# Kernel tuning notes

Hardware: AMD Instinct MI355X
Metric: run time of the kernel (lower is better)

## Reference

```python
import jax, jax.numpy as jnp
import numpy as np
from functools import reduce

# 6x6 open-boundary PEPS, bond dim D=4, physical dim 2, boundary contraction
# from ymin with projector compression to CHI=8, projectors perturbed by a
# 2-layer MLP of the spin configuration (eta = 1e-3), then full contraction.
Lx, Ly, D, PHYS = 6, 6, 4, 2
CHI = 8
NHID = 64
ETA = 1e-3
NSITES = Lx * Ly
BATCH = 1024


def _proj_shapes():
    # Static propagation of projector tensor shapes (mirrors the sweep below).
    u = [1] + [D] * (Lx - 1)
    d = [D] * (Lx - 1) + [1]
    shapes = []
    for j in range(1, Ly - 1):
        nu = [u[i] * (1 if i == 0 else D) for i in range(Lx)]
        nd = [d[i] * (1 if i == Lx - 1 else D) for i in range(Lx)]
        for i in range(Lx - 1):
            m = nd[i]
            k1 = min(nu[i] * D, m)
            k2 = min(D * nd[i + 1], m)
            cb = min(CHI, k1, k2)
            shapes += [(m, cb), (m, cb)]
            nd[i] = cb
            nu[i + 1] = cb
        u, d = nu, nd
    return shapes


PROJ_SHAPES = _proj_shapes()
PROJ_LEN = sum(m * c for m, c in PROJ_SHAPES)  # == 6400


def _site(T, xi, i, j):
    # select physical index; axes of result: (up, right, down, left)
    t = jnp.take(T[i, j], xi[i * Ly + j], axis=-1)
    if i == 0:
        t = t[:1]          # lattice top edge: up bond is trivial
    if i == Lx - 1:
        t = t[:, :, :1]    # lattice bottom edge: down bond is trivial
    return t


def _sweep(A, projs):
    # boundary MPS from column 0; B[i] axes: (u, r, d)
    B = [A[i][0][:, :, :, 0] for i in range(Lx)]
    out = [] if projs is None else None
    p = 0
    for j in range(1, Ly - 1):
        Bn = []
        for i in range(Lx):
            t = A[i][j]  # (a, R, b, l)
            nt = jnp.einsum('uxd,aRbx->uaRdb', B[i], t)
            u_, a_, R_, d_, b_ = nt.shape
            Bn.append(nt.reshape(u_ * a_, R_, d_ * b_))
        for i in range(Lx - 1):
            Tt, Tb = Bn[i], Bn[i + 1]
            m = Tt.shape[-1]
            if projs is None:
                mt = Tt.reshape(-1, m)        # (ut*R, m)
                mb = Tb.reshape(m, -1)        # (m, R*db)
                R1 = jnp.linalg.qr(mt, mode='r')     # (k1, m)
                R2 = jnp.linalg.qr(mb.T, mode='r')   # (k2, m)
                U, S, Vh = jnp.linalg.svd(R1 @ R2.T, full_matrices=False)
                cb = min(CHI, S.shape[-1])
                sinv = 1.0 / jnp.sqrt(S[:cb] + 1e-12)
                Pd = (R2.T @ Vh[:cb].T) * sinv  # (m, cb): top tensor's down bond
                Pu = (R1.T @ U[:, :cb]) * sinv  # (m, cb): bottom tensor's up bond
                out += [Pd, Pu]
            else:
                Pd, Pu = projs[p], projs[p + 1]
                p += 2
            Bn[i] = jnp.einsum('uRm,mc->uRc', Tt, Pd)
            Bn[i + 1] = jnp.einsum('mRd,mc->cRd', Tb, Pu)
        B = Bn
    return B, out


def _finalize(B, A):
    Cs = []
    for i in range(Lx):
        t = A[i][Ly - 1][:, 0]  # (a, b, l): right bond is trivial
        c = jnp.einsum('uxd,abx->uadb', B[i], t)
        ua, aa, dd, bb = c.shape
        Cs.append(c.reshape(ua * aa, dd * bb))
    return reduce(jnp.matmul, Cs)[0, 0]


def _mlp(xf, W1, b1, W2, b2):
    h = jax.nn.relu(xf @ W1.T + b1)
    return h @ W2.T + b2


def _amp_single(T, W1, b1, W2, b2, xi):
    A = [[_site(T, xi, i, j) for j in range(Ly)] for i in range(Lx)]
    # pass 1: compute data-dependent projectors
    _, plist = _sweep(A, None)
    vec = jnp.concatenate([pp.reshape(-1) for pp in plist])
    vec = vec + _mlp(xi.astype(jnp.float32), W1, b1, W2, b2) * ETA
    # unpack perturbed projectors
    newp, ptr = [], 0
    for pp in plist:
        n = pp.size
        newp.append(vec[ptr:ptr + n].reshape(pp.shape))
        ptr += n
    # pass 2: contract the full network with the perturbed projectors
    B, _ = _sweep(A, newp)
    return _finalize(B, A)


def setup_inputs() -> dict:
    key = jax.random.key(0)
    ks = jax.random.split(key, 6)
    T = jax.random.normal(ks[0], (Lx, Ly, D, D, D, D, PHYS), dtype=jnp.float32) * 0.5
    W1 = jax.random.normal(ks[1], (NHID, NSITES), dtype=jnp.float32) / np.sqrt(NSITES).astype(np.float32)
    b1 = jnp.zeros((NHID,), dtype=jnp.float32)
    W2 = jax.random.normal(ks[2], (PROJ_LEN, NHID), dtype=jnp.float32) / np.sqrt(NHID).astype(np.float32)
    b2 = jnp.zeros((PROJ_LEN,), dtype=jnp.float32)
    x = jax.random.randint(ks[3], (BATCH, NSITES), 0, PHYS, dtype=jnp.int32)
    return {"T": T, "W1": W1, "b1": b1, "W2": W2, "b2": b2, "x": x}


def reference(T, W1, b1, W2, b2, x):
    return jax.vmap(lambda xi: _amp_single(T, W1, b1, W2, b2, xi))(x)
```

## Files before the change

kernel.cpp:

```cpp
#include <hip/hip_runtime.h>

#define BS 256

__device__ const int g_uprev[2][6] = {{1,4,4,4,4,4},{1,4,8,8,8,4}};
__device__ const int g_dprev[2][6] = {{4,4,4,4,4,1},{4,8,8,8,4,1}};
__device__ const int g_mtab[2][5]  = {{16,16,16,16,16},{16,32,32,32,16}};
__device__ const int g_cbtab[5]    = {4,8,8,8,4};
__device__ const int g_ucurtab[5]  = {1,4,8,8,8};
__device__ const int g_dntab[2][5] = {{16,16,16,16,1},{32,32,32,16,1}};
__device__ const int g_path[2][5]  = {{0,0,1,1,2},{0,0,0,0,2}};
__device__ const int g_offtab[4][5]= {{0,128,384,640,896},
                                      {1024,1152,1664,2176,2688},
                                      {2816,2944,3456,3968,4480},
                                      {4608,4736,5248,5760,6272}};
__device__ const int g_ufin[6] = {1,4,8,8,8,4};
__device__ const int g_dfin[6] = {4,8,8,8,4,1};

__global__ __launch_bounds__(256) void mlp_kernel(
    const float* __restrict__ W1, const float* __restrict__ b1,
    const float* __restrict__ W2, const float* __restrict__ b2,
    const int* __restrict__ x, float* __restrict__ proj)
{
  __shared__ float hbuf[8][64];
  const int tid = threadIdx.x;
  const int s0 = blockIdx.x << 3;
  for (int e = tid; e < 512; e += 256) {
    const int sl = e >> 6, hh = e & 63;
    const int* xr = x + (s0 + sl) * 36;
    const float* wr = W1 + hh * 36;
    float acc = b1[hh];
    #pragma unroll
    for (int t = 0; t < 36; ++t) acc += wr[t] * (float)xr[t];
    hbuf[sl][hh] = fmaxf(acc, 0.0f);
  }
  __syncthreads();
  for (int k = tid; k < 6400; k += 256) {
    const float4* wr = (const float4*)(W2 + (size_t)k * 64);
    float acc[8];
    #pragma unroll
    for (int s2 = 0; s2 < 8; ++s2) acc[s2] = 0.0f;
    #pragma unroll
    for (int c = 0; c < 16; ++c) {
      const float4 w = wr[c];
      #pragma unroll
      for (int s2 = 0; s2 < 8; ++s2) {
        const float4 hv = ((const float4*)hbuf[s2])[c];
        acc[s2] += w.x * hv.x + w.y * hv.y + w.z * hv.z + w.w * hv.w;
      }
    }
    const float bb = b2[k];
    #pragma unroll
    for (int s2 = 0; s2 < 8; ++s2)
      proj[(size_t)(s0 + s2) * 6400 + k] = 0.001f * (acc[s2] + bb);
  }
}

__device__ __forceinline__ void jrot(float app, float aqq, float apq, float& c, float& sn) {
  c = 1.0f; sn = 0.0f;
  if (fabsf(apq) > 1e-36f + 1e-12f * (fabsf(app) + fabsf(aqq))) {
    const float tau = (aqq - app) * 0.5f * __builtin_amdgcn_rcpf(apq);
    const float t = copysignf(1.0f, tau) *
                    __builtin_amdgcn_rcpf(fabsf(tau) + __builtin_amdgcn_sqrtf(1.0f + tau * tau));
    c = __builtin_amdgcn_rsqf(1.0f + t * t);
    sn = t * c;
  }
}

__device__ __forceinline__ int seatof(int i, int n) {
  return (i == n - 1) ? 0 : ((i == 0) ? 1 : ((i < (n >> 1)) ? (2 * i) : (2 * (n - 1 - i) + 1)));
}

__device__ __forceinline__ int sgshift(int s, int np) {
  if (s == 0) return 0;
  if (s & 1) return (s == 2 * np - 1) ? (2 * np - 2) : (s + 2);
  return (s == 2) ? 1 : (s - 2);
}

template<int N>
__device__ void jacobi_pb(float* __restrict__ H, float* __restrict__ V, int tid)
{
  constexpr int NP = N / 2;
  constexpr int NM1 = N - 1;
  constexpr int NL = (N == 32) ? 5 : ((N == 16) ? 4 : 2);
  constexpr int NVMAX = (N == 32) ? 2 : 1;
  constexpr int MAXSW = (N == 32) ? 5 : ((N == 16) ? 5 : 3);
  for (int e = tid; e < N * N; e += BS) {
    const int r = e >> NL, c = e & (N - 1);
    const int i0 = (c == 0) ? NM1 : ((c == 1) ? 0 : ((c & 1) ? (NM1 - (c >> 1)) : (c >> 1)));
    V[r * 36 + c] = (r == i0) ? 1.0f : 0.0f;
  }
  __syncthreads();
  const int cp = tid & (NP - 1);
  const bool hact = (N == 32) ? true : ((N == 16) ? (tid < 64) : (tid < 4));
  const bool vact = (N == 32) ? true : ((N == 16) ? (tid < 128) : (tid < 8));
  const int q0 = 2 * cp, q1 = q0 + 1;
  const int d0 = sgshift(q0, NP), d1 = sgshift(q1, NP);
  const int rt = (N == 32) ? (tid >> 4) : ((N == 16) ? (tid >> 3) : (tid >> 1));
  const int r0 = 2 * rt, r1 = r0 + 1;
  const int e0 = sgshift(r0, NP), e1 = sgshift(r1, NP);
  int vr[NVMAX];
  #pragma unroll
  for (int vi = 0; vi < NVMAX; ++vi)
    vr[vi] = ((N == 32) ? (tid >> 4) : ((N == 16) ? (tid >> 3) : (tid >> 1))) + NP * vi;

  for (int sw = 0; sw < MAXSW; ++sw) {
    for (int rd = 0; rd < NM1; ++rd) {
      const float2 dg = *(const float2*)(H + q0 * 36 + q0);
      const float aqq = H[q1 * 36 + q1];
      float cc_, cs_;
      jrot(dg.x, aqq, dg.y, cc_, cs_);
      float o00, o01, o10, o11;
      if (hact) {
        const float cr_ = __shfl(cc_, rt);
        const float sr_ = __shfl(cs_, rt);
        const float2 rA = *(const float2*)(H + r0 * 36 + q0);
        const float2 rB = *(const float2*)(H + r1 * 36 + q0);
        const float t1 = cr_ * rA.x - sr_ * rB.x, t2 = cr_ * rA.y - sr_ * rB.y;
        const float u1 = sr_ * rA.x + cr_ * rB.x, u2 = sr_ * rA.y + cr_ * rB.y;
        o00 = cc_ * t1 - cs_ * t2; o01 = cs_ * t1 + cc_ * t2;
        o10 = cc_ * u1 - cs_ * u2; o11 = cs_ * u1 + cc_ * u2;
      }
      float v0[NVMAX], v1[NVMAX];
      #pragma unroll
      for (int vi = 0; vi < NVMAX; ++vi) {
        if (vi == 0 && !vact) continue;
        const float2 vv = *(const float2*)(V + vr[vi] * 36 + q0);
        v0[vi] = cc_ * vv.x - cs_ * vv.y;
        v1[vi] = cs_ * vv.x + cc_ * vv.y;
      }
      __syncthreads();
      if (hact) {
        H[e0 * 36 + d0] = o00; H[e0 * 36 + d1] = o01;
        H[e1 * 36 + d0] = o10; H[e1 * 36 + d1] = o11;
      }
      #pragma unroll
      for (int vi = 0; vi < NVMAX; ++vi) {
        if (vi == 0 && !vact) continue;
        V[vr[vi] * 36 + d0] = v0[vi];
        V[vr[vi] * 36 + d1] = v1[vi];
      }
      __syncthreads();
    }
  }
}

__device__ __forceinline__ void gram_cols(float* __restrict__ G, const float* __restrict__ A,
                                          int nrows, int mcols, bool init, int tid)
{
  const int q4 = mcols >> 2;
  const int q4log = (mcols == 32) ? 3 : 2;
  const int nel = mcols * q4;
  const float4* A4 = (const float4*)A;
  float4* G4 = (float4*)G;
  for (int e = tid; e < nel; e += BS) {
    const int c2q = e & (q4 - 1);
    const int c1 = e >> q4log;
    float ax = 0.f, ay = 0.f, az = 0.f, aw = 0.f;
    for (int r = 0; r < nrows; ++r) {
      const float a1 = A[r * 36 + c1];
      const float4 a2 = A4[r * 9 + c2q];
      ax += a1 * a2.x; ay += a1 * a2.y; az += a1 * a2.z; aw += a1 * a2.w;
    }
    float4* gp = G4 + c1 * 9 + c2q;
    if (init) { float4 o; o.x = ax; o.y = ay; o.z = az; o.w = aw; *gp = o; }
    else { float4 o = *gp; o.x += ax; o.y += ay; o.z += az; o.w += aw; *gp = o; }
  }
  __syncthreads();
}

__device__ __forceinline__ void absorb_T(const float* __restrict__ Tg, const float* __restrict__ poolS,
    float* __restrict__ BIGT, float* __restrict__ ATile, const int* __restrict__ xi,
    int i1, int j, int U, int Dd, int rr0, int rr1, int tid)
{
  const int bd = (i1 == 5) ? 1 : 4;
  const int dbw = Dd * bd;
  const int mt_ = U * 4;
  const int ph = xi[i1 * 6 + j];
  const float* tb = Tg + (size_t)(i1 * 6 + j) * 512;
  for (int e = tid; e < 256; e += BS) ATile[e] = tb[e * 2 + ph];
  __syncthreads();
  const int mlog = (mt_ == 32) ? 5 : 4;
  const int dblog = 31 - __clz(dbw);
  const int bdlog = (bd == 4) ? 2 : 0;
  const int nel = mt_ * dbw * (rr1 - rr0);
  for (int e = tid; e < nel; e += BS) {
    const int ua = e & (mt_ - 1);
    const int db = (e >> mlog) & (dbw - 1);
    const int rr = rr0 + (e >> (mlog + dblog));
    const int u = ua >> 2, a = ua & 3;
    const int d_ = db >> bdlog, b = db & (bd - 1);
    const float* op = poolS + u * 33 + d_;
    const float4 av = *(const float4*)(ATile + a * 64 + rr * 16 + b * 4);
    BIGT[((rr - rr0) * dbw + db) * 36 + ua] = op[0] * av.x + op[8] * av.y + op[16] * av.z + op[24] * av.w;
  }
  __syncthreads();
}

__global__ __launch_bounds__(256, 4) void peps_kernel(
    const float* __restrict__ Tg, const int* __restrict__ x,
    float* __restrict__ proj, float* __restrict__ out)
{
  __shared__ __align__(16) float pool[6 * 264];
  __shared__ __align__(16) float CUR[1152];
  __shared__ __align__(16) float BIGT[2304];
  __shared__ __align__(16) float GbM[1152];
  __shared__ __align__(16) float TM[1152];
  __shared__ __align__(16) float GM[1152];
  __shared__ __align__(16) float ATile[256];
  __shared__ __align__(16) float PdL[256], PuL[256];
  __shared__ float red[4];
  __shared__ int isel[8];
  __shared__ float sinvv[8], sdiv[8];
  __shared__ int xi[36];
  __shared__ float vvec[36], vvec2[36];

  const int s = blockIdx.x;
  const int tid = threadIdx.x;
  if (tid < 36) xi[tid] = x[s * 36 + tid];
  __syncthreads();

  for (int sweep = 0; sweep < 2; ++sweep) {
    for (int i2 = 0; i2 < 6; ++i2) {
      const int ad = (i2 == 0) ? 1 : 4, bd = (i2 == 5) ? 1 : 4;
      const int bdlog = (bd == 4) ? 2 : 0;
      const int ph = xi[i2 * 6];
      const float* tb = Tg + (size_t)(i2 * 6) * 512;
      const int nel = ad * 4 * bd;
      for (int e = tid; e < nel; e += BS) {
        const int b = e & (bd - 1);
        const int rr = (e >> bdlog) & 3;
        const int a = e >> (bdlog + 2);
        pool[i2 * 264 + a * 33 + rr * 8 + b] = tb[(a * 64 + rr * 16 + b * 4) * 2 + ph];
      }
    }
    __syncthreads();

    for (int j = 1; j <= 4; ++j) {
      const int jj = (j > 1) ? 1 : 0;
      {
        const int ph = xi[j];
        const float* tb = Tg + (size_t)j * 512;
        for (int e = tid; e < 256; e += BS) ATile[e] = tb[e * 2 + ph];
        __syncthreads();
        for (int e = tid; e < 64; e += BS) {
          const int db = e & 15;
          const int rr = e >> 4;
          const int d_ = db >> 2, b = db & 3;
          const float* op = pool + d_;
          const float4 av = *(const float4*)(ATile + rr * 16 + b * 4);
          CUR[rr * 36 + db] = op[0] * av.x + op[8] * av.y + op[16] * av.z + op[24] * av.w;
        }
        __syncthreads();
      }

      for (int i = 0; i < 5; ++i) {
        const int m = g_mtab[jj][i], cb = g_cbtab[i], ucur = g_ucurtab[i], dn = g_dntab[jj][i];
        const int p = ucur * 4, path = g_path[jj][i];
        const int U1 = g_uprev[jj][i + 1], Dd1 = g_dprev[jj][i + 1];
        const bool two = (dn == 32);
        const int cblog = (cb == 8) ? 3 : 2;
        const int mq4 = m >> 2;
        float* projb = proj + (size_t)s * 6400 + g_offtab[j - 1][i];

        if (sweep == 0) {
          if (path == 2) {
            absorb_T(Tg, pool + (i + 1) * 264, BIGT, ATile, xi, i + 1, j, U1, Dd1, 0, 4, tid);
            gram_cols(GbM, CUR, p, m, true, tid);
            for (int e = tid; e < 64; e += BS) {
              const int r = e & 3, k = e >> 2;
              float acc = 0.f;
              const float4* G4 = (const float4*)GbM;
              const float4* B4 = (const float4*)BIGT;
              for (int lq = 0; lq < 4; ++lq) {
                const float4 g = G4[k * 9 + lq], b = B4[r * 9 + lq];
                acc += g.x * b.x + g.y * b.y + g.z * b.z + g.w * b.w;
              }
              TM[k * 36 + r] = acc;
            }
            __syncthreads();
            for (int e = tid; e < 16; e += BS) {
              const int c = e & 3, r = e >> 2;
              float acc = 0.f;
              for (int k = 0; k < 16; ++k) acc += BIGT[r * 36 + k] * TM[k * 36 + c];
              GM[seatof(r, 4) * 36 + seatof(c, 4)] = acc;
            }
            __syncthreads();
            jacobi_pb<4>(GM, TM + 576, tid);
          } else if (path == 0) {
            if (!two) {
              absorb_T(Tg, pool + (i + 1) * 264, BIGT, ATile, xi, i + 1, j, U1, Dd1, 0, 4, tid);
              gram_cols(GbM, BIGT, 4 * dn, m, true, tid);
            } else {
              absorb_T(Tg, pool + (i + 1) * 264, BIGT, ATile, xi, i + 1, j, U1, Dd1, 0, 2, tid);
              gram_cols(GbM, BIGT, 2 * dn, m, true, tid);
              absorb_T(Tg, pool + (i + 1) * 264, BIGT, ATile, xi, i + 1, j, U1, Dd1, 2, 4, tid);
              gram_cols(GbM, BIGT, 2 * dn, m, false, tid);
            }
            const int q4log = (m == 32) ? 3 : 2;
            for (int e = tid; e < p * mq4; e += BS) {
              const int lq = e & (mq4 - 1), pr = e >> q4log;
              float ax = 0.f, ay = 0.f, az = 0.f, aw = 0.f;
              const float4* G4 = (const float4*)GbM;
              for (int k = 0; k < m; ++k) {
                const float a1 = CUR[pr * 36 + k];
                const float4 g = G4[k * 9 + lq];
                ax += a1 * g.x; ay += a1 * g.y; az += a1 * g.z; aw += a1 * g.w;
              }
              float4 o; o.x = ax; o.y = ay; o.z = az; o.w = aw;
              ((float4*)TM)[pr * 9 + lq] = o;
            }
            __syncthreads();
            const int plog = (p == 32) ? 5 : ((p == 16) ? 4 : 2);
            for (int e = tid; e < p * p; e += BS) {
              const int pc = e & (p - 1), pr = e >> plog;
              float acc = 0.f;
              const float4* T4 = (const float4*)TM;
              const float4* C4 = (const float4*)CUR;
              for (int lq = 0; lq < mq4; ++lq) {
                const float4 t = T4[pr * 9 + lq], c = C4[pc * 9 + lq];
                acc += t.x * c.x + t.y * c.y + t.z * c.z + t.w * c.w;
              }
              GM[seatof(pr, p) * 36 + seatof(pc, p)] = acc;
            }
            __syncthreads();
            if (p == 4)       jacobi_pb<4>(GM, TM, tid);
            else if (p == 16) jacobi_pb<16>(GM, TM, tid);
            else              jacobi_pb<32>(GM, TM, tid);
          } else {
            absorb_T(Tg, pool + (i + 1) * 264, BIGT, ATile, xi, i + 1, j, U1, Dd1, 0, 4, tid);
            gram_cols(GbM + 576, CUR, p, m, true, tid);
            gram_cols(GbM, BIGT, 4 * dn, m, true, tid);
            if (tid < 64) {
              float v_ = (tid < 16) ? GbM[tid * 37] : -3.0e38f;
              for (int mk = 32; mk; mk >>= 1) v_ = fmaxf(v_, __shfl_xor(v_, mk));
              if (tid == 0) red[0] = v_;
            }
            __syncthreads();
            const float thr = 1e-10f * red[0] + 1e-35f;
            for (int k = 0; k < 16; ++k) {
              const float dk = GbM[k * 37];
              const float rs = (dk > thr) ? (1.0f / sqrtf(dk)) : 0.0f;
              if (tid < 16) TM[k * 36 + tid] = GbM[k * 36 + tid] * rs;
              __syncthreads();
              const int rows = 15 - k;
              for (int e = tid; e < rows * 16; e += BS) {
                const int ii = k + 1 + (e >> 4), jc = e & 15;
                GbM[ii * 36 + jc] -= TM[k * 36 + ii] * TM[k * 36 + jc];
              }
              __syncthreads();
            }
            for (int e = tid; e < 64; e += BS) {
              const int jq = e & 3, k = e >> 2;
              float ax = 0.f, ay = 0.f, az = 0.f, aw = 0.f;
              const float4* Gt4 = (const float4*)(GbM + 576);
              for (int l = 0; l < 16; ++l) {
                const float r2 = TM[k * 36 + l];
                const float4 g = Gt4[l * 9 + jq];
                ax += r2 * g.x; ay += r2 * g.y; az += r2 * g.z; aw += r2 * g.w;
              }
              float4 o; o.x = ax; o.y = ay; o.z = az; o.w = aw;
              ((float4*)(TM + 576))[k * 9 + jq] = o;
            }
            __syncthreads();
            for (int e = tid; e < 256; e += BS) {
              const int k2 = e & 15, k = e >> 4;
              float acc = 0.f;
              const float4* T14 = (const float4*)(TM + 576);
              const float4* R24 = (const float4*)TM;
              for (int lq = 0; lq < 4; ++lq) {
                const float4 t = T14[k * 9 + lq], r = R24[k2 * 9 + lq];
                acc += t.x * r.x + t.y * r.y + t.z * r.z + t.w * r.w;
              }
              GM[seatof(k, 16) * 36 + seatof(k2, 16)] = acc;
            }
            __syncthreads();
            jacobi_pb<16>(GM, TM + 576, tid);
          }

          const int N = (path == 2) ? 4 : ((path == 1) ? 16 : p);
          if (tid < 64) {
            float v_ = (tid < N) ? GM[tid * 37] : -3.0e38f;
            int ix = tid;
            for (int t = 0; t < cb; ++t) {
              float bv = v_; int bi = ix;
              for (int mk = 32; mk; mk >>= 1) {
                const float ov = __shfl_xor(bv, mk);
                const int oi = __shfl_xor(bi, mk);
                if (ov > bv || (ov == bv && oi < bi)) { bv = ov; bi = oi; }
              }
              if (tid == 0) isel[t] = bi;
              if (ix == bi) v_ = -3.0e38f;
            }
          }
          __syncthreads();
          if (tid < cb) {
            const float lam = GM[isel[tid] * 37];
            const float s_ = sqrtf(fmaxf(lam, 0.0f));
            sinvv[tid] = 1.0f / sqrtf(s_ + 1e-12f);
            sdiv[tid]  = 1.0f / fmaxf(s_, 1e-25f);
          }
          __syncthreads();

          if (path == 0) {
            for (int e = tid; e < m * cb; e += BS) {
              const int k = e & (cb - 1), mrow = e >> cblog;
              const int a = isel[k];
              float acc = 0.f;
              for (int pr = 0; pr < p; ++pr) acc += CUR[pr * 36 + mrow] * TM[pr * 36 + a];
              PuL[mrow * 8 + k] = acc * sinvv[k];
            }
            __syncthreads();
            for (int e = tid; e < m * cb; e += BS) {
              const int k = e & (cb - 1), mrow = e >> cblog;
              float acc = 0.f;
              for (int l = 0; l < m; ++l) acc += GbM[mrow * 36 + l] * PuL[l * 8 + k];
              PdL[mrow * 8 + k] = acc * sdiv[k];
            }
            __syncthreads();
          } else if (path == 2) {
            for (int e = tid; e < m * cb; e += BS) {
              const int k = e & (cb - 1), mrow = e >> cblog;
              const int a = isel[k];
              float acc = 0.f;
              for (int r = 0; r < 4; ++r) acc += BIGT[r * 36 + mrow] * TM[576 + r * 36 + a];
              PdL[mrow * 8 + k] = acc * sinvv[k];
            }
            __syncthreads();
            for (int e = tid; e < m * cb; e += BS) {
              const int k = e & (cb - 1), mrow = e >> cblog;
              float acc = 0.f;
              for (int l = 0; l < m; ++l) acc += GbM[mrow * 36 + l] * PdL[l * 8 + k];
              PuL[mrow * 8 + k] = acc * sdiv[k];
            }
            __syncthreads();
          } else {
            for (int e = tid; e < m * cb; e += BS) {
              const int k = e & (cb - 1), mrow = e >> cblog;
              const int a = isel[k];
              float acc = 0.f;
              for (int t = 0; t < 16; ++t) acc += TM[t * 36 + mrow] * TM[576 + t * 36 + a];
              PdL[mrow * 8 + k] = acc * sinvv[k];
            }
            __syncthreads();
            for (int e = tid; e < m * cb; e += BS) {
              const int k = e & (cb - 1), mrow = e >> cblog;
              float acc = 0.f;
              for (int l = 0; l < m; ++l) acc += GbM[576 + mrow * 36 + l] * PdL[l * 8 + k];
              PuL[mrow * 8 + k] = acc * sdiv[k];
            }
            __syncthreads();
          }
          for (int e = tid; e < m * cb; e += BS)
            projb[e] += PdL[(e >> cblog) * 8 + (e & (cb - 1))];
          for (int e = tid; e < m * cb; e += BS)
            projb[m * cb + e] += PuL[(e >> cblog) * 8 + (e & (cb - 1))];
        } else {
          for (int e = tid; e < m * cb; e += BS)
            PdL[(e >> cblog) * 8 + (e & (cb - 1))] = projb[e];
          for (int e = tid; e < m * cb; e += BS)
            PuL[(e >> cblog) * 8 + (e & (cb - 1))] = projb[m * cb + e];
          __syncthreads();
          if (!two) absorb_T(Tg, pool + (i + 1) * 264, BIGT, ATile, xi, i + 1, j, U1, Dd1, 0, 4, tid);
          else      absorb_T(Tg, pool + (i + 1) * 264, BIGT, ATile, xi, i + 1, j, U1, Dd1, 2, 4, tid);
        }

        {
          const int nel = ucur * 4 * cb;
          const float4* C4 = (const float4*)CUR;
          for (int e = tid; e < nel; e += BS) {
            const int cc = e & (cb - 1);
            const int rr = (e >> cblog) & 3;
            const int u = e >> (cblog + 2);
            const int row = u * 4 + rr;
            float acc = 0.f;
            for (int mq = 0; mq < mq4; ++mq) {
              const float4 cv = C4[row * 9 + mq];
              acc += cv.x * PdL[(mq * 4 + 0) * 8 + cc] + cv.y * PdL[(mq * 4 + 1) * 8 + cc]
                   + cv.z * PdL[(mq * 4 + 2) * 8 + cc] + cv.w * PdL[(mq * 4 + 3) * 8 + cc];
            }
            pool[i * 264 + u * 33 + rr * 8 + cc] = acc;
          }
          __syncthreads();

          const int dnlog = 31 - __clz(dn);
          auto bn1 = [&](int rr0, int nloc) {
            const int ne2 = cb * nloc * dn;
            const float4* B4 = (const float4*)BIGT;
            for (int e = tid; e < ne2; e += BS) {
              const int dd = e & (dn - 1);
              const int t = e >> dnlog;
              const int rrL = t & (nloc - 1);
              const int cc = t >> ((nloc == 4) ? 2 : 1);
              const int row = rrL * dn + dd;
              float acc = 0.f;
              for (int mq = 0; mq < mq4; ++mq) {
                const float4 bv = B4[row * 9 + mq];
                acc += bv.x * PuL[(mq * 4 + 0) * 8 + cc] + bv.y * PuL[(mq * 4 + 1) * 8 + cc]
                     + bv.z * PuL[(mq * 4 + 2) * 8 + cc] + bv.w * PuL[(mq * 4 + 3) * 8 + cc];
              }
              if (i < 4) CUR[(cc * 4 + rr0 + rrL) * 36 + dd] = acc;
              else       pool[5 * 264 + cc * 33 + (rr0 + rrL) * 8] = acc;
            }
            __syncthreads();
          };
          if (!two) {
            bn1(0, 4);
          } else {
            bn1(2, 2);
            absorb_T(Tg, pool + (i + 1) * 264, BIGT, ATile, xi, i + 1, j, U1, Dd1, 0, 2, tid);
            bn1(0, 2);
          }
        }
      }
    }

    if (sweep == 1) {
      if (tid == 0) vvec[0] = 1.0f;
      __syncthreads();
      for (int i = 0; i < 6; ++i) {
        const int ad = (i == 0) ? 1 : 4, bd = (i == 5) ? 1 : 4;
        const int adlog = (ad == 4) ? 2 : 0, bdlog = (bd == 4) ? 2 : 0;
        const int rows = g_ufin[i] * ad, cols = g_dfin[i] * bd;
        const int clog = 31 - __clz(cols);
        const int ph = xi[i * 6 + 5];
        const float* tb = Tg + (size_t)(i * 6 + 5) * 512;
        for (int e = tid; e < 256; e += BS) ATile[e] = tb[e * 2 + ph];
        __syncthreads();
        for (int e = tid; e < rows * cols; e += BS) {
          const int col = e & (cols - 1);
          const int ua = e >> clog;
          const int u = ua >> adlog, a = ua & (ad - 1);
          const int d_ = col >> bdlog, b = col & (bd - 1);
          const float* fb = pool + i * 264 + u * 33 + d_;
          const float4 av = *(const float4*)(ATile + a * 64 + b * 4);
          GM[ua * 36 + col] = fb[0] * av.x + fb[8] * av.y + fb[16] * av.z + fb[24] * av.w;
        }
        __syncthreads();
        if (tid < cols) {
          float acc = 0.f;
          for (int r_ = 0; r_ < rows; ++r_) acc += vvec[r_] * GM[r_ * 36 + tid];
          vvec2[tid] = acc;
        }
        __syncthreads();
        if (tid < cols) vvec[tid] = vvec2[tid];
        __syncthreads();
      }
      if (tid == 0) out[s] = vvec[0];
    }
  }
}

extern "C" void kernel_launch(void* const* d_in, const int* in_sizes, int n_in,
                              void* d_out, int out_size, void* d_ws, size_t ws_size,
                              hipStream_t stream) {
  const float* Tg = (const float*)d_in[0];
  const float* W1 = (const float*)d_in[1];
  const float* b1 = (const float*)d_in[2];
  const float* W2 = (const float*)d_in[3];
  const float* b2 = (const float*)d_in[4];
  const int*   x  = (const int*)d_in[5];
  float* out = (float*)d_out;
  float* proj = (float*)d_ws;
  (void)in_sizes; (void)n_in; (void)out_size; (void)ws_size;

  mlp_kernel<<<dim3(128), dim3(256), 0, stream>>>(W1, b1, W2, b2, x, proj);
  peps_kernel<<<dim3(1024), dim3(256), 0, stream>>>(Tg, x, proj, out);
}
```

Baseline: 1.360 ms.

## Process two samples per block to amortize barriers and fill idle lanes

```diff
diff --git a/kernel.cpp b/kernel.cpp
--- a/kernel.cpp
+++ b/kernel.cpp
@@ -1,6 +1,9 @@
 #include <hip/hip_runtime.h>
 
 #define BS 256
+#define SS 1152
+#define PSS 1584
+#define BSS 2304
 
 __device__ const int g_uprev[2][6] = {{1,4,4,4,4,4},{1,4,8,8,8,4}};
 __device__ const int g_dprev[2][6] = {{4,4,4,4,4,1},{4,8,8,8,4,1}};
@@ -69,7 +72,6 @@
 __device__ __forceinline__ int seatof(int i, int n) {
   return (i == n - 1) ? 0 : ((i == 0) ? 1 : ((i < (n >> 1)) ? (2 * i) : (2 * (n - 1 - i) + 1)));
 }
-
 __device__ __forceinline__ int sgshift(int s, int np) {
   if (s == 0) return 0;
   if (s & 1) return (s == 2 * np - 1) ? (2 * np - 2) : (s + 2);
@@ -77,91 +79,140 @@
 }
 
 template<int N>
-__device__ void jacobi_pb(float* __restrict__ H, float* __restrict__ V, int tid)
+__device__ void jacobi_pb(float* __restrict__ Hb, float* __restrict__ Vb, int tid)
 {
   constexpr int NP = N / 2;
   constexpr int NM1 = N - 1;
   constexpr int NL = (N == 32) ? 5 : ((N == 16) ? 4 : 2);
-  constexpr int NVMAX = (N == 32) ? 2 : 1;
   constexpr int MAXSW = (N == 32) ? 5 : ((N == 16) ? 5 : 3);
-  for (int e = tid; e < N * N; e += BS) {
+  for (int e2 = tid; e2 < 2 * N * N; e2 += BS) {
+    const int sm = (e2 >= N * N) ? 1 : 0;
+    const int e = e2 - sm * N * N;
     const int r = e >> NL, c = e & (N - 1);
     const int i0 = (c == 0) ? NM1 : ((c == 1) ? 0 : ((c & 1) ? (NM1 - (c >> 1)) : (c >> 1)));
-    V[r * 36 + c] = (r == i0) ? 1.0f : 0.0f;
+    Vb[sm * SS + r * 36 + c] = (r == i0) ? 1.0f : 0.0f;
   }
   __syncthreads();
   const int cp = tid & (NP - 1);
-  const bool hact = (N == 32) ? true : ((N == 16) ? (tid < 64) : (tid < 4));
-  const bool vact = (N == 32) ? true : ((N == 16) ? (tid < 128) : (tid < 8));
   const int q0 = 2 * cp, q1 = q0 + 1;
   const int d0 = sgshift(q0, NP), d1 = sgshift(q1, NP);
-  const int rt = (N == 32) ? (tid >> 4) : ((N == 16) ? (tid >> 3) : (tid >> 1));
-  const int r0 = 2 * rt, r1 = r0 + 1;
-  const int e0 = sgshift(r0, NP), e1 = sgshift(r1, NP);
-  int vr[NVMAX];
-  #pragma unroll
-  for (int vi = 0; vi < NVMAX; ++vi)
-    vr[vi] = ((N == 32) ? (tid >> 4) : ((N == 16) ? (tid >> 3) : (tid >> 1))) + NP * vi;
-
-  for (int sw = 0; sw < MAXSW; ++sw) {
-    for (int rd = 0; rd < NM1; ++rd) {
-      const float2 dg = *(const float2*)(H + q0 * 36 + q0);
-      const float aqq = H[q1 * 36 + q1];
-      float cc_, cs_;
-      jrot(dg.x, aqq, dg.y, cc_, cs_);
-      float o00, o01, o10, o11;
-      if (hact) {
-        const float cr_ = __shfl(cc_, rt);
-        const float sr_ = __shfl(cs_, rt);
-        const float2 rA = *(const float2*)(H + r0 * 36 + q0);
-        const float2 rB = *(const float2*)(H + r1 * 36 + q0);
-        const float t1 = cr_ * rA.x - sr_ * rB.x, t2 = cr_ * rA.y - sr_ * rB.y;
-        const float u1 = sr_ * rA.x + cr_ * rB.x, u2 = sr_ * rA.y + cr_ * rB.y;
-        o00 = cc_ * t1 - cs_ * t2; o01 = cs_ * t1 + cc_ * t2;
-        o10 = cc_ * u1 - cs_ * u2; o11 = cs_ * u1 + cc_ * u2;
+
+  if (N == 32) {
+    const int rt = tid >> 4;
+    const int r0 = 2 * rt, r1 = r0 + 1;
+    const int e0 = sgshift(r0, NP), e1 = sgshift(r1, NP);
+    const int vrow0 = rt, vrow1 = rt + 16;
+    for (int sw = 0; sw < MAXSW; ++sw)
+      for (int rd = 0; rd < NM1; ++rd) {
+        float c0, s0, c1, s1;
+        { const float2 dg = *(const float2*)(Hb + q0 * 36 + q0);
+          jrot(dg.x, Hb[q1 * 36 + q1], dg.y, c0, s0); }
+        { const float2 dg = *(const float2*)(Hb + SS + q0 * 36 + q0);
+          jrot(dg.x, Hb[SS + q1 * 36 + q1], dg.y, c1, s1); }
+        const float cr0 = __shfl(c0, rt), sr0 = __shfl(s0, rt);
+        const float cr1 = __shfl(c1, rt), sr1 = __shfl(s1, rt);
+        float o[2][4], va[2][2], vb[2][2];
+        #pragma unroll
+        for (int sm = 0; sm < 2; ++sm) {
+          const float cc_ = sm ? c1 : c0, cs_ = sm ? s1 : s0;
+          const float cr_ = sm ? cr1 : cr0, sr_ = sm ? sr1 : sr0;
+          const float* H = Hb + sm * SS;
+          const float2 rA = *(const float2*)(H + r0 * 36 + q0);
+          const float2 rB = *(const float2*)(H + r1 * 36 + q0);
+          const float t1 = cr_ * rA.x - sr_ * rB.x, t2 = cr_ * rA.y - sr_ * rB.y;
+          const float u1 = sr_ * rA.x + cr_ * rB.x, u2 = sr_ * rA.y + cr_ * rB.y;
+          o[sm][0] = cc_ * t1 - cs_ * t2; o[sm][1] = cs_ * t1 + cc_ * t2;
+          o[sm][2] = cc_ * u1 - cs_ * u2; o[sm][3] = cs_ * u1 + cc_ * u2;
+          const float* V = Vb + sm * SS;
+          const float2 v0 = *(const float2*)(V + vrow0 * 36 + q0);
+          const float2 v1 = *(const float2*)(V + vrow1 * 36 + q0);
+          va[sm][0] = cc_ * v0.x - cs_ * v0.y; va[sm][1] = cs_ * v0.x + cc_ * v0.y;
+          vb[sm][0] = cc_ * v1.x - cs_ * v1.y; vb[sm][1] = cs_ * v1.x + cc_ * v1.y;
+        }
+        __syncthreads();
+        #pragma unroll
+        for (int sm = 0; sm < 2; ++sm) {
+          float* H = Hb + sm * SS;
+          H[e0 * 36 + d0] = o[sm][0]; H[e0 * 36 + d1] = o[sm][1];
+          H[e1 * 36 + d0] = o[sm][2]; H[e1 * 36 + d1] = o[sm][3];
+          float* V = Vb + sm * SS;
+          V[vrow0 * 36 + d0] = va[sm][0]; V[vrow0 * 36 + d1] = va[sm][1];
+          V[vrow1 * 36 + d0] = vb[sm][0]; V[vrow1 * 36 + d1] = vb[sm][1];
+        }
+        __syncthreads();
       }
-      float v0[NVMAX], v1[NVMAX];
-      #pragma unroll
-      for (int vi = 0; vi < NVMAX; ++vi) {
-        if (vi == 0 && !vact) continue;
-        const float2 vv = *(const float2*)(V + vr[vi] * 36 + q0);
-        v0[vi] = cc_ * vv.x - cs_ * vv.y;
-        v1[vi] = cs_ * vv.x + cc_ * vv.y;
+  } else {
+    const int hsm = (N == 16) ? ((tid >> 6) & 1) : ((tid >> 2) & 1);
+    const bool hact = (N == 16) ? (tid < 128) : (tid < 8);
+    const int rt = (N == 16) ? ((tid >> 3) & 7) : ((tid >> 1) & 1);
+    const int r0 = 2 * rt, r1 = r0 + 1;
+    const int e0 = sgshift(r0, NP), e1 = sgshift(r1, NP);
+    const int vsm = (N == 16) ? (tid >> 7) : ((tid >> 3) & 1);
+    const bool vact = (N == 16) ? true : (tid < 16);
+    const int vrow = (N == 16) ? ((tid >> 3) & 15) : ((tid >> 1) & 3);
+    for (int sw = 0; sw < MAXSW; ++sw)
+      for (int rd = 0; rd < NM1; ++rd) {
+        float c0, s0, c1, s1;
+        { const float2 dg = *(const float2*)(Hb + q0 * 36 + q0);
+          jrot(dg.x, Hb[q1 * 36 + q1], dg.y, c0, s0); }
+        { const float2 dg = *(const float2*)(Hb + SS + q0 * 36 + q0);
+          jrot(dg.x, Hb[SS + q1 * 36 + q1], dg.y, c1, s1); }
+        const float cr0 = __shfl(c0, rt), sr0 = __shfl(s0, rt);
+        const float cr1 = __shfl(c1, rt), sr1 = __shfl(s1, rt);
+        float o0, o1, o2, o3, w0, w1;
+        if (hact) {
+          const float cc_ = hsm ? c1 : c0, cs_ = hsm ? s1 : s0;
+          const float cr_ = hsm ? cr1 : cr0, sr_ = hsm ? sr1 : sr0;
+          const float* H = Hb + hsm * SS;
+          const float2 rA = *(const float2*)(H + r0 * 36 + q0);
+          const float2 rB = *(const float2*)(H + r1 * 36 + q0);
+          const float t1 = cr_ * rA.x - sr_ * rB.x, t2 = cr_ * rA.y - sr_ * rB.y;
+          const float u1 = sr_ * rA.x + cr_ * rB.x, u2 = sr_ * rA.y + cr_ * rB.y;
+          o0 = cc_ * t1 - cs_ * t2; o1 = cs_ * t1 + cc_ * t2;
+          o2 = cc_ * u1 - cs_ * u2; o3 = cs_ * u1 + cc_ * u2;
+        }
+        if (vact) {
+          const float cc_ = vsm ? c1 : c0, cs_ = vsm ? s1 : s0;
+          const float2 vv = *(const float2*)(Vb + vsm * SS + vrow * 36 + q0);
+          w0 = cc_ * vv.x - cs_ * vv.y;
+          w1 = cs_ * vv.x + cc_ * vv.y;
+        }
+        __syncthreads();
+        if (hact) {
+          float* H = Hb + hsm * SS;
+          H[e0 * 36 + d0] = o0; H[e0 * 36 + d1] = o1;
+          H[e1 * 36 + d0] = o2; H[e1 * 36 + d1] = o3;
+        }
+        if (vact) {
+          float* V = Vb + vsm * SS;
+          V[vrow * 36 + d0] = w0;
+          V[vrow * 36 + d1] = w1;
+        }
+        __syncthreads();
       }
-      __syncthreads();
-      if (hact) {
-        H[e0 * 36 + d0] = o00; H[e0 * 36 + d1] = o01;
-        H[e1 * 36 + d0] = o10; H[e1 * 36 + d1] = o11;
-      }
-      #pragma unroll
-      for (int vi = 0; vi < NVMAX; ++vi) {
-        if (vi == 0 && !vact) continue;
-        V[vr[vi] * 36 + d0] = v0[vi];
-        V[vr[vi] * 36 + d1] = v1[vi];
-      }
-      __syncthreads();
-    }
   }
 }
 
 __device__ __forceinline__ void gram_cols(float* __restrict__ G, const float* __restrict__ A,
-                                          int nrows, int mcols, bool init, int tid)
+                                          int as_, int nrows, int mcols, bool init, int tid)
 {
   const int q4 = mcols >> 2;
   const int q4log = (mcols == 32) ? 3 : 2;
   const int nel = mcols * q4;
-  const float4* A4 = (const float4*)A;
-  float4* G4 = (float4*)G;
-  for (int e = tid; e < nel; e += BS) {
+  for (int e2 = tid; e2 < 2 * nel; e2 += BS) {
+    const int sm = (e2 >= nel) ? 1 : 0;
+    const int e = e2 - sm * nel;
+    const float* As = A + sm * as_;
+    float* Gs = G + sm * SS;
     const int c2q = e & (q4 - 1);
     const int c1 = e >> q4log;
     float ax = 0.f, ay = 0.f, az = 0.f, aw = 0.f;
     for (int r = 0; r < nrows; ++r) {
-      const float a1 = A[r * 36 + c1];
-      const float4 a2 = A4[r * 9 + c2q];
+      const float a1 = As[r * 36 + c1];
+      const float4 a2 = *(const float4*)(As + r * 36 + c2q * 4);
       ax += a1 * a2.x; ay += a1 * a2.y; az += a1 * a2.z; aw += a1 * a2.w;
     }
-    float4* gp = G4 + c1 * 9 + c2q;
+    float4* gp = (float4*)(Gs + c1 * 36 + c2q * 4);
     if (init) { float4 o; o.x = ax; o.y = ay; o.z = az; o.w = aw; *gp = o; }
     else { float4 o = *gp; o.x += ax; o.y += ay; o.z += az; o.w += aw; *gp = o; }
   }
@@ -175,62 +226,69 @@
   const int bd = (i1 == 5) ? 1 : 4;
   const int dbw = Dd * bd;
   const int mt_ = U * 4;
-  const int ph = xi[i1 * 6 + j];
   const float* tb = Tg + (size_t)(i1 * 6 + j) * 512;
-  for (int e = tid; e < 256; e += BS) ATile[e] = tb[e * 2 + ph];
+  for (int e2 = tid; e2 < 512; e2 += BS) {
+    const int sm = e2 >> 8, e = e2 & 255;
+    ATile[sm * 256 + e] = tb[e * 2 + xi[sm * 36 + i1 * 6 + j]];
+  }
   __syncthreads();
   const int mlog = (mt_ == 32) ? 5 : 4;
   const int dblog = 31 - __clz(dbw);
   const int bdlog = (bd == 4) ? 2 : 0;
   const int nel = mt_ * dbw * (rr1 - rr0);
-  for (int e = tid; e < nel; e += BS) {
+  for (int e2 = tid; e2 < 2 * nel; e2 += BS) {
+    const int sm = (e2 >= nel) ? 1 : 0;
+    const int e = e2 - sm * nel;
     const int ua = e & (mt_ - 1);
     const int db = (e >> mlog) & (dbw - 1);
     const int rr = rr0 + (e >> (mlog + dblog));
     const int u = ua >> 2, a = ua & 3;
     const int d_ = db >> bdlog, b = db & (bd - 1);
-    const float* op = poolS + u * 33 + d_;
-    const float4 av = *(const float4*)(ATile + a * 64 + rr * 16 + b * 4);
-    BIGT[((rr - rr0) * dbw + db) * 36 + ua] = op[0] * av.x + op[8] * av.y + op[16] * av.z + op[24] * av.w;
+    const float* op = poolS + sm * PSS + u * 33 + d_;
+    const float4 av = *(const float4*)(ATile + sm * 256 + a * 64 + rr * 16 + b * 4);
+    BIGT[sm * BSS + ((rr - rr0) * dbw + db) * 36 + ua] =
+        op[0] * av.x + op[8] * av.y + op[16] * av.z + op[24] * av.w;
   }
   __syncthreads();
 }
 
-__global__ __launch_bounds__(256, 4) void peps_kernel(
+__global__ __launch_bounds__(256, 2) void peps_kernel(
     const float* __restrict__ Tg, const int* __restrict__ x,
     float* __restrict__ proj, float* __restrict__ out)
 {
-  __shared__ __align__(16) float pool[6 * 264];
-  __shared__ __align__(16) float CUR[1152];
-  __shared__ __align__(16) float BIGT[2304];
-  __shared__ __align__(16) float GbM[1152];
-  __shared__ __align__(16) float TM[1152];
-  __shared__ __align__(16) float GM[1152];
-  __shared__ __align__(16) float ATile[256];
-  __shared__ __align__(16) float PdL[256], PuL[256];
-  __shared__ float red[4];
-  __shared__ int isel[8];
-  __shared__ float sinvv[8], sdiv[8];
-  __shared__ int xi[36];
-  __shared__ float vvec[36], vvec2[36];
-
-  const int s = blockIdx.x;
+  __shared__ __align__(16) float pool[2 * PSS];
+  __shared__ __align__(16) float CUR[2 * SS];
+  __shared__ __align__(16) float BIGT[2 * BSS];
+  __shared__ __align__(16) float GbM[2 * SS];
+  __shared__ __align__(16) float TM[2 * SS];
+  __shared__ __align__(16) float GM[2 * SS];
+  __shared__ __align__(16) float ATile[2 * 256];
+  __shared__ __align__(16) float PdL[2 * 256], PuL[2 * 256];
+  __shared__ float red[2];
+  __shared__ int isel[2 * 8];
+  __shared__ float sinvv[2 * 8], sdiv[2 * 8];
+  __shared__ int xi[2 * 36];
+  __shared__ float vvec[2 * 36], vvec2[2 * 36];
+
+  const int s0 = blockIdx.x * 2;
   const int tid = threadIdx.x;
-  if (tid < 36) xi[tid] = x[s * 36 + tid];
+  if (tid < 72) xi[tid] = x[s0 * 36 + tid];
   __syncthreads();
 
   for (int sweep = 0; sweep < 2; ++sweep) {
     for (int i2 = 0; i2 < 6; ++i2) {
       const int ad = (i2 == 0) ? 1 : 4, bd = (i2 == 5) ? 1 : 4;
       const int bdlog = (bd == 4) ? 2 : 0;
-      const int ph = xi[i2 * 6];
       const float* tb = Tg + (size_t)(i2 * 6) * 512;
       const int nel = ad * 4 * bd;
-      for (int e = tid; e < nel; e += BS) {
+      for (int e2 = tid; e2 < 2 * nel; e2 += BS) {
+        const int sm = (e2 >= nel) ? 1 : 0;
+        const int e = e2 - sm * nel;
+        const int ph = xi[sm * 36 + i2 * 6];
         const int b = e & (bd - 1);
         const int rr = (e >> bdlog) & 3;
         const int a = e >> (bdlog + 2);
-        pool[i2 * 264 + a * 33 + rr * 8 + b] = tb[(a * 64 + rr * 16 + b * 4) * 2 + ph];
+        pool[sm * PSS + i2 * 264 + a * 33 + rr * 8 + b] = tb[(a * 64 + rr * 16 + b * 4) * 2 + ph];
       }
     }
     __syncthreads();
@@ -238,17 +296,20 @@
     for (int j = 1; j <= 4; ++j) {
       const int jj = (j > 1) ? 1 : 0;
       {
-        const int ph = xi[j];
         const float* tb = Tg + (size_t)j * 512;
-        for (int e = tid; e < 256; e += BS) ATile[e] = tb[e * 2 + ph];
-        __syncthreads();
-        for (int e = tid; e < 64; e += BS) {
-          const int db = e & 15;
-          const int rr = e >> 4;
+        for (int e2 = tid; e2 < 512; e2 += BS) {
+          const int sm = e2 >> 8, e = e2 & 255;
+          ATile[sm * 256 + e] = tb[e * 2 + xi[sm * 36 + j]];
+        }
+        __syncthreads();
+        for (int e2 = tid; e2 < 128; e2 += BS) {
+          const int sm = e2 >= 64 ? 1 : 0;
+          const int e = e2 & 63;
+          const int db = e & 15, rr = e >> 4;
           const int d_ = db >> 2, b = db & 3;
-          const float* op = pool + d_;
-          const float4 av = *(const float4*)(ATile + rr * 16 + b * 4);
-          CUR[rr * 36 + db] = op[0] * av.x + op[8] * av.y + op[16] * av.z + op[24] * av.w;
+          const float* op = pool + sm * PSS + d_;
+          const float4 av = *(const float4*)(ATile + sm * 256 + rr * 16 + b * 4);
+          CUR[sm * SS + rr * 36 + db] = op[0] * av.x + op[8] * av.y + op[16] * av.z + op[24] * av.w;
         }
         __syncthreads();
       }
@@ -260,67 +321,75 @@
         const bool two = (dn == 32);
         const int cblog = (cb == 8) ? 3 : 2;
         const int mq4 = m >> 2;
-        float* projb = proj + (size_t)s * 6400 + g_offtab[j - 1][i];
+        const int offv = g_offtab[j - 1][i];
 
         if (sweep == 0) {
           if (path == 2) {
             absorb_T(Tg, pool + (i + 1) * 264, BIGT, ATile, xi, i + 1, j, U1, Dd1, 0, 4, tid);
-            gram_cols(GbM, CUR, p, m, true, tid);
-            for (int e = tid; e < 64; e += BS) {
+            gram_cols(GbM, CUR, SS, p, m, true, tid);
+            for (int e2 = tid; e2 < 128; e2 += BS) {
+              const int sm = e2 >= 64 ? 1 : 0;
+              const int e = e2 & 63;
               const int r = e & 3, k = e >> 2;
               float acc = 0.f;
-              const float4* G4 = (const float4*)GbM;
-              const float4* B4 = (const float4*)BIGT;
               for (int lq = 0; lq < 4; ++lq) {
-                const float4 g = G4[k * 9 + lq], b = B4[r * 9 + lq];
+                const float4 g = *(const float4*)(GbM + sm * SS + k * 36 + lq * 4);
+                const float4 b = *(const float4*)(BIGT + sm * BSS + r * 36 + lq * 4);
                 acc += g.x * b.x + g.y * b.y + g.z * b.z + g.w * b.w;
               }
-              TM[k * 36 + r] = acc;
-            }
-            __syncthreads();
-            for (int e = tid; e < 16; e += BS) {
+              TM[sm * SS + k * 36 + r] = acc;
+            }
+            __syncthreads();
+            for (int e2 = tid; e2 < 32; e2 += BS) {
+              const int sm = e2 >= 16 ? 1 : 0;
+              const int e = e2 & 15;
               const int c = e & 3, r = e >> 2;
               float acc = 0.f;
-              for (int k = 0; k < 16; ++k) acc += BIGT[r * 36 + k] * TM[k * 36 + c];
-              GM[seatof(r, 4) * 36 + seatof(c, 4)] = acc;
+              for (int k = 0; k < 16; ++k)
+                acc += BIGT[sm * BSS + r * 36 + k] * TM[sm * SS + k * 36 + c];
+              GM[sm * SS + seatof(r, 4) * 36 + seatof(c, 4)] = acc;
             }
             __syncthreads();
             jacobi_pb<4>(GM, TM + 576, tid);
           } else if (path == 0) {
             if (!two) {
               absorb_T(Tg, pool + (i + 1) * 264, BIGT, ATile, xi, i + 1, j, U1, Dd1, 0, 4, tid);
-              gram_cols(GbM, BIGT, 4 * dn, m, true, tid);
+              gram_cols(GbM, BIGT, BSS, 4 * dn, m, true, tid);
             } else {
               absorb_T(Tg, pool + (i + 1) * 264, BIGT, ATile, xi, i + 1, j, U1, Dd1, 0, 2, tid);
-              gram_cols(GbM, BIGT, 2 * dn, m, true, tid);
+              gram_cols(GbM, BIGT, BSS, 2 * dn, m, true, tid);
               absorb_T(Tg, pool + (i + 1) * 264, BIGT, ATile, xi, i + 1, j, U1, Dd1, 2, 4, tid);
-              gram_cols(GbM, BIGT, 2 * dn, m, false, tid);
+              gram_cols(GbM, BIGT, BSS, 2 * dn, m, false, tid);
             }
             const int q4log = (m == 32) ? 3 : 2;
-            for (int e = tid; e < p * mq4; e += BS) {
+            const int nel1 = p * mq4;
+            for (int e2 = tid; e2 < 2 * nel1; e2 += BS) {
+              const int sm = (e2 >= nel1) ? 1 : 0;
+              const int e = e2 - sm * nel1;
               const int lq = e & (mq4 - 1), pr = e >> q4log;
               float ax = 0.f, ay = 0.f, az = 0.f, aw = 0.f;
-              const float4* G4 = (const float4*)GbM;
               for (int k = 0; k < m; ++k) {
-                const float a1 = CUR[pr * 36 + k];
-                const float4 g = G4[k * 9 + lq];
+                const float a1 = CUR[sm * SS + pr * 36 + k];
+                const float4 g = *(const float4*)(GbM + sm * SS + k * 36 + lq * 4);
                 ax += a1 * g.x; ay += a1 * g.y; az += a1 * g.z; aw += a1 * g.w;
               }
               float4 o; o.x = ax; o.y = ay; o.z = az; o.w = aw;
-              ((float4*)TM)[pr * 9 + lq] = o;
+              *(float4*)(TM + sm * SS + pr * 36 + lq * 4) = o;
             }
             __syncthreads();
             const int plog = (p == 32) ? 5 : ((p == 16) ? 4 : 2);
-            for (int e = tid; e < p * p; e += BS) {
+            const int nel2 = p * p;
+            for (int e2 = tid; e2 < 2 * nel2; e2 += BS) {
+              const int sm = (e2 >= nel2) ? 1 : 0;
+              const int e = e2 - sm * nel2;
               const int pc = e & (p - 1), pr = e >> plog;
               float acc = 0.f;
-              const float4* T4 = (const float4*)TM;
-              const float4* C4 = (const float4*)CUR;
               for (int lq = 0; lq < mq4; ++lq) {
-                const float4 t = T4[pr * 9 + lq], c = C4[pc * 9 + lq];
+                const float4 t = *(const float4*)(TM + sm * SS + pr * 36 + lq * 4);
+                const float4 c = *(const float4*)(CUR + sm * SS + pc * 36 + lq * 4);
                 acc += t.x * c.x + t.y * c.y + t.z * c.z + t.w * c.w;
               }
-              GM[seatof(pr, p) * 36 + seatof(pc, p)] = acc;
+              GM[sm * SS + seatof(pr, p) * 36 + seatof(pc, p)] = acc;
             }
             __syncthreads();
             if (p == 4)       jacobi_pb<4>(GM, TM, tid);
@@ -328,59 +397,68 @@
             else              jacobi_pb<32>(GM, TM, tid);
           } else {
             absorb_T(Tg, pool + (i + 1) * 264, BIGT, ATile, xi, i + 1, j, U1, Dd1, 0, 4, tid);
-            gram_cols(GbM + 576, CUR, p, m, true, tid);
-            gram_cols(GbM, BIGT, 4 * dn, m, true, tid);
-            if (tid < 64) {
-              float v_ = (tid < 16) ? GbM[tid * 37] : -3.0e38f;
+            gram_cols(GbM + 576, CUR, SS, p, m, true, tid);
+            gram_cols(GbM, BIGT, BSS, 4 * dn, m, true, tid);
+            if (tid < 128) {
+              const int sm = tid >> 6, l = tid & 63;
+              float v_ = (l < 16) ? GbM[sm * SS + l * 37] : -3.0e38f;
               for (int mk = 32; mk; mk >>= 1) v_ = fmaxf(v_, __shfl_xor(v_, mk));
-              if (tid == 0) red[0] = v_;
-            }
-            __syncthreads();
-            const float thr = 1e-10f * red[0] + 1e-35f;
+              if (l == 0) red[sm] = v_;
+            }
+            __syncthreads();
             for (int k = 0; k < 16; ++k) {
-              const float dk = GbM[k * 37];
-              const float rs = (dk > thr) ? (1.0f / sqrtf(dk)) : 0.0f;
-              if (tid < 16) TM[k * 36 + tid] = GbM[k * 36 + tid] * rs;
+              if (tid < 32) {
+                const int sm = tid >> 4, col = tid & 15;
+                const float thr = 1e-10f * red[sm] + 1e-35f;
+                const float dk = GbM[sm * SS + k * 37];
+                const float rs = (dk > thr) ? (1.0f / sqrtf(dk)) : 0.0f;
+                TM[sm * SS + k * 36 + col] = GbM[sm * SS + k * 36 + col] * rs;
+              }
               __syncthreads();
               const int rows = 15 - k;
-              for (int e = tid; e < rows * 16; e += BS) {
+              for (int e2 = tid; e2 < 2 * rows * 16; e2 += BS) {
+                const int sm = (e2 >= rows * 16) ? 1 : 0;
+                const int e = e2 - sm * rows * 16;
                 const int ii = k + 1 + (e >> 4), jc = e & 15;
-                GbM[ii * 36 + jc] -= TM[k * 36 + ii] * TM[k * 36 + jc];
+                GbM[sm * SS + ii * 36 + jc] -= TM[sm * SS + k * 36 + ii] * TM[sm * SS + k * 36 + jc];
               }
               __syncthreads();
             }
-            for (int e = tid; e < 64; e += BS) {
+            for (int e2 = tid; e2 < 128; e2 += BS) {
+              const int sm = e2 >= 64 ? 1 : 0;
+              const int e = e2 & 63;
               const int jq = e & 3, k = e >> 2;
               float ax = 0.f, ay = 0.f, az = 0.f, aw = 0.f;
-              const float4* Gt4 = (const float4*)(GbM + 576);
               for (int l = 0; l < 16; ++l) {
-                const float r2 = TM[k * 36 + l];
-                const float4 g = Gt4[l * 9 + jq];
+                const float r2 = TM[sm * SS + k * 36 + l];
+                const float4 g = *(const float4*)(GbM + sm * SS + 576 + l * 36 + jq * 4);
                 ax += r2 * g.x; ay += r2 * g.y; az += r2 * g.z; aw += r2 * g.w;
               }
               float4 o; o.x = ax; o.y = ay; o.z = az; o.w = aw;
-              ((float4*)(TM + 576))[k * 9 + jq] = o;
-            }
-            __syncthreads();
-            for (int e = tid; e < 256; e += BS) {
+              *(float4*)(TM + sm * SS + 576 + k * 36 + jq * 4) = o;
+            }
+            __syncthreads();
+            for (int e2 = tid; e2 < 512; e2 += BS) {
+              const int sm = e2 >= 256 ? 1 : 0;
+              const int e = e2 & 255;
               const int k2 = e & 15, k = e >> 4;
               float acc = 0.f;
-              const float4* T14 = (const float4*)(TM + 576);
-              const float4* R24 = (const float4*)TM;
               for (int lq = 0; lq < 4; ++lq) {
-                const float4 t = T14[k * 9 + lq], r = R24[k2 * 9 + lq];
+                const float4 t = *(const float4*)(TM + sm * SS + 576 + k * 36 + lq * 4);
+                const float4 r = *(const float4*)(TM + sm * SS + k2 * 36 + lq * 4);
                 acc += t.x * r.x + t.y * r.y + t.z * r.z + t.w * r.w;
               }
-              GM[seatof(k, 16) * 36 + seatof(k2, 16)] = acc;
+              GM[sm * SS + seatof(k, 16) * 36 + seatof(k2, 16)] = acc;
             }
             __syncthreads();
             jacobi_pb<16>(GM, TM + 576, tid);
           }
 
           const int N = (path == 2) ? 4 : ((path == 1) ? 16 : p);
-          if (tid < 64) {
-            float v_ = (tid < N) ? GM[tid * 37] : -3.0e38f;
-            int ix = tid;
+          if (tid < 128) {
+            const int sm = tid >> 6, l = tid & 63;
+            float v_ = (l < N) ? GM[sm * SS + l * 37] : -3.0e38f;
+            int ix = l;
             for (int t = 0; t < cb; ++t) {
               float bv = v_; int bi = ix;
               for (int mk = 32; mk; mk >>= 1) {
@@ -388,77 +466,111 @@
                 const int oi = __shfl_xor(bi, mk);
                 if (ov > bv || (ov == bv && oi < bi)) { bv = ov; bi = oi; }
               }
-              if (tid == 0) isel[t] = bi;
+              if (l == 0) isel[sm * 8 + t] = bi;
               if (ix == bi) v_ = -3.0e38f;
             }
           }
           __syncthreads();
-          if (tid < cb) {
-            const float lam = GM[isel[tid] * 37];
+          if (tid < 2 * cb) {
+            const int sm = (tid >= cb) ? 1 : 0;
+            const int k = tid - sm * cb;
+            const float lam = GM[sm * SS + isel[sm * 8 + k] * 37];
             const float s_ = sqrtf(fmaxf(lam, 0.0f));
-            sinvv[tid] = 1.0f / sqrtf(s_ + 1e-12f);
-            sdiv[tid]  = 1.0f / fmaxf(s_, 1e-25f);
+            sinvv[sm * 8 + k] = 1.0f / sqrtf(s_ + 1e-12f);
+            sdiv[sm * 8 + k] = 1.0f / fmaxf(s_, 1e-25f);
           }
           __syncthreads();
 
+          const int mcb = m * cb;
           if (path == 0) {
-            for (int e = tid; e < m * cb; e += BS) {
+            for (int e2 = tid; e2 < 2 * mcb; e2 += BS) {
+              const int sm = (e2 >= mcb) ? 1 : 0;
+              const int e = e2 - sm * mcb;
               const int k = e & (cb - 1), mrow = e >> cblog;
-              const int a = isel[k];
-              float acc = 0.f;
-              for (int pr = 0; pr < p; ++pr) acc += CUR[pr * 36 + mrow] * TM[pr * 36 + a];
-              PuL[mrow * 8 + k] = acc * sinvv[k];
-            }
-            __syncthreads();
-            for (int e = tid; e < m * cb; e += BS) {
+              const int a = isel[sm * 8 + k];
+              float acc = 0.f;
+              for (int pr = 0; pr < p; ++pr)
+                acc += CUR[sm * SS + pr * 36 + mrow] * TM[sm * SS + pr * 36 + a];
+              PuL[sm * 256 + mrow * 8 + k] = acc * sinvv[sm * 8 + k];
+            }
+            __syncthreads();
+            for (int e2 = tid; e2 < 2 * mcb; e2 += BS) {
+              const int sm = (e2 >= mcb) ? 1 : 0;
+              const int e = e2 - sm * mcb;
               const int k = e & (cb - 1), mrow = e >> cblog;
               float acc = 0.f;
-              for (int l = 0; l < m; ++l) acc += GbM[mrow * 36 + l] * PuL[l * 8 + k];
-              PdL[mrow * 8 + k] = acc * sdiv[k];
+              for (int l = 0; l < m; ++l)
+                acc += GbM[sm * SS + mrow * 36 + l] * PuL[sm * 256 + l * 8 + k];
+              PdL[sm * 256 + mrow * 8 + k] = acc * sdiv[sm * 8 + k];
             }
             __syncthreads();
           } else if (path == 2) {
-            for (int e = tid; e < m * cb; e += BS) {
+            for (int e2 = tid; e2 < 2 * mcb; e2 += BS) {
+              const int sm = (e2 >= mcb) ? 1 : 0;
+              const int e = e2 - sm * mcb;
               const int k = e & (cb - 1), mrow = e >> cblog;
-              const int a = isel[k];
-              float acc = 0.f;
-              for (int r = 0; r < 4; ++r) acc += BIGT[r * 36 + mrow] * TM[576 + r * 36 + a];
-              PdL[mrow * 8 + k] = acc * sinvv[k];
-            }
-            __syncthreads();
-            for (int e = tid; e < m * cb; e += BS) {
+              const int a = isel[sm * 8 + k];
+              float acc = 0.f;
+              for (int r = 0; r < 4; ++r)
+                acc += BIGT[sm * BSS + r * 36 + mrow] * TM[sm * SS + 576 + r * 36 + a];
+              PdL[sm * 256 + mrow * 8 + k] = acc * sinvv[sm * 8 + k];
+            }
+            __syncthreads();
+            for (int e2 = tid; e2 < 2 * mcb; e2 += BS) {
+              const int sm = (e2 >= mcb) ? 1 : 0;
+              const int e = e2 - sm * mcb;
               const int k = e & (cb - 1), mrow = e >> cblog;
               float acc = 0.f;
-              for (int l = 0; l < m; ++l) acc += GbM[mrow * 36 + l] * PdL[l * 8 + k];
-              PuL[mrow * 8 + k] = acc * sdiv[k];
+              for (int l = 0; l < m; ++l)
+                acc += GbM[sm * SS + mrow * 36 + l] * PdL[sm * 256 + l * 8 + k];
+              PuL[sm * 256 + mrow * 8 + k] = acc * sdiv[sm * 8 + k];
             }
             __syncthreads();
           } else {
-            for (int e = tid; e < m * cb; e += BS) {
+            for (int e2 = tid; e2 < 2 * mcb; e2 += BS) {
+              const int sm = (e2 >= mcb) ? 1 : 0;
+              const int e = e2 - sm * mcb;
               const int k = e & (cb - 1), mrow = e >> cblog;
-              const int a = isel[k];
-              float acc = 0.f;
-              for (int t = 0; t < 16; ++t) acc += TM[t * 36 + mrow] * TM[576 + t * 36 + a];
-              PdL[mrow * 8 + k] = acc * sinvv[k];
-            }
-            __syncthreads();
-            for (int e = tid; e < m * cb; e += BS) {
+              const int a = isel[sm * 8 + k];
+              float acc = 0.f;
+              for (int t = 0; t < 16; ++t)
+                acc += TM[sm * SS + t * 36 + mrow] * TM[sm * SS + 576 + t * 36 + a];
+              PdL[sm * 256 + mrow * 8 + k] = acc * sinvv[sm * 8 + k];
+            }
+            __syncthreads();
+            for (int e2 = tid; e2 < 2 * mcb; e2 += BS) {
+              const int sm = (e2 >= mcb) ? 1 : 0;
+              const int e = e2 - sm * mcb;
               const int k = e & (cb - 1), mrow = e >> cblog;
               float acc = 0.f;
-              for (int l = 0; l < m; ++l) acc += GbM[576 + mrow * 36 + l] * PdL[l * 8 + k];
-              PuL[mrow * 8 + k] = acc * sdiv[k];
-            }
-            __syncthreads();
-          }
-          for (int e = tid; e < m * cb; e += BS)
-            projb[e] += PdL[(e >> cblog) * 8 + (e & (cb - 1))];
-          for (int e = tid; e < m * cb; e += BS)
-            projb[m * cb + e] += PuL[(e >> cblog) * 8 + (e & (cb - 1))];
+              for (int l = 0; l < m; ++l)
+                acc += GbM[sm * SS + 576 + mrow * 36 + l] * PdL[sm * 256 + l * 8 + k];
+              PuL[sm * 256 + mrow * 8 + k] = acc * sdiv[sm * 8 + k];
+            }
+            __syncthreads();
+          }
+          for (int e2 = tid; e2 < 2 * mcb; e2 += BS) {
+            const int sm = (e2 >= mcb) ? 1 : 0;
+            const int e = e2 - sm * mcb;
+            proj[(size_t)(s0 + sm) * 6400 + offv + e] += PdL[sm * 256 + (e >> cblog) * 8 + (e & (cb - 1))];
+          }
+          for (int e2 = tid; e2 < 2 * mcb; e2 += BS) {
+            const int sm = (e2 >= mcb) ? 1 : 0;
+            const int e = e2 - sm * mcb;
+            proj[(size_t)(s0 + sm) * 6400 + offv + mcb + e] += PuL[sm * 256 + (e >> cblog) * 8 + (e & (cb - 1))];
+          }
         } else {
-          for (int e = tid; e < m * cb; e += BS)
-            PdL[(e >> cblog) * 8 + (e & (cb - 1))] = projb[e];
-          for (int e = tid; e < m * cb; e += BS)
-            PuL[(e >> cblog) * 8 + (e & (cb - 1))] = projb[m * cb + e];
+          const int mcb = m * cb;
+          for (int e2 = tid; e2 < 2 * mcb; e2 += BS) {
+            const int sm = (e2 >= mcb) ? 1 : 0;
+            const int e = e2 - sm * mcb;
+            PdL[sm * 256 + (e >> cblog) * 8 + (e & (cb - 1))] = proj[(size_t)(s0 + sm) * 6400 + offv + e];
+          }
+          for (int e2 = tid; e2 < 2 * mcb; e2 += BS) {
+            const int sm = (e2 >= mcb) ? 1 : 0;
+            const int e = e2 - sm * mcb;
+            PuL[sm * 256 + (e >> cblog) * 8 + (e & (cb - 1))] = proj[(size_t)(s0 + sm) * 6400 + offv + mcb + e];
+          }
           __syncthreads();
           if (!two) absorb_T(Tg, pool + (i + 1) * 264, BIGT, ATile, xi, i + 1, j, U1, Dd1, 0, 4, tid);
           else      absorb_T(Tg, pool + (i + 1) * 264, BIGT, ATile, xi, i + 1, j, U1, Dd1, 2, 4, tid);
@@ -466,27 +578,29 @@
 
         {
           const int nel = ucur * 4 * cb;
-          const float4* C4 = (const float4*)CUR;
-          for (int e = tid; e < nel; e += BS) {
+          for (int e2 = tid; e2 < 2 * nel; e2 += BS) {
+            const int sm = (e2 >= nel) ? 1 : 0;
+            const int e = e2 - sm * nel;
             const int cc = e & (cb - 1);
             const int rr = (e >> cblog) & 3;
             const int u = e >> (cblog + 2);
             const int row = u * 4 + rr;
             float acc = 0.f;
             for (int mq = 0; mq < mq4; ++mq) {
-              const float4 cv = C4[row * 9 + mq];
-              acc += cv.x * PdL[(mq * 4 + 0) * 8 + cc] + cv.y * PdL[(mq * 4 + 1) * 8 + cc]
-                   + cv.z * PdL[(mq * 4 + 2) * 8 + cc] + cv.w * PdL[(mq * 4 + 3) * 8 + cc];
-            }
-            pool[i * 264 + u * 33 + rr * 8 + cc] = acc;
+              const float4 cv = *(const float4*)(CUR + sm * SS + row * 36 + mq * 4);
+              acc += cv.x * PdL[sm * 256 + (mq * 4 + 0) * 8 + cc] + cv.y * PdL[sm * 256 + (mq * 4 + 1) * 8 + cc]
+                   + cv.z * PdL[sm * 256 + (mq * 4 + 2) * 8 + cc] + cv.w * PdL[sm * 256 + (mq * 4 + 3) * 8 + cc];
+            }
+            pool[sm * PSS + i * 264 + u * 33 + rr * 8 + cc] = acc;
           }
           __syncthreads();
 
           const int dnlog = 31 - __clz(dn);
           auto bn1 = [&](int rr0, int nloc) {
             const int ne2 = cb * nloc * dn;
-            const float4* B4 = (const float4*)BIGT;
-            for (int e = tid; e < ne2; e += BS) {
+            for (int e2 = tid; e2 < 2 * ne2; e2 += BS) {
+              const int sm = (e2 >= ne2) ? 1 : 0;
+              const int e = e2 - sm * ne2;
               const int dd = e & (dn - 1);
               const int t = e >> dnlog;
               const int rrL = t & (nloc - 1);
@@ -494,12 +608,12 @@
               const int row = rrL * dn + dd;
               float acc = 0.f;
               for (int mq = 0; mq < mq4; ++mq) {
-                const float4 bv = B4[row * 9 + mq];
-                acc += bv.x * PuL[(mq * 4 + 0) * 8 + cc] + bv.y * PuL[(mq * 4 + 1) * 8 + cc]
-                     + bv.z * PuL[(mq * 4 + 2) * 8 + cc] + bv.w * PuL[(mq * 4 + 3) * 8 + cc];
-              }
-              if (i < 4) CUR[(cc * 4 + rr0 + rrL) * 36 + dd] = acc;
-              else       pool[5 * 264 + cc * 33 + (rr0 + rrL) * 8] = acc;
+                const float4 bv = *(const float4*)(BIGT + sm * BSS + row * 36 + mq * 4);
+                acc += bv.x * PuL[sm * 256 + (mq * 4 + 0) * 8 + cc] + bv.y * PuL[sm * 256 + (mq * 4 + 1) * 8 + cc]
+                     + bv.z * PuL[sm * 256 + (mq * 4 + 2) * 8 + cc] + bv.w * PuL[sm * 256 + (mq * 4 + 3) * 8 + cc];
+              }
+              if (i < 4) CUR[sm * SS + (cc * 4 + rr0 + rrL) * 36 + dd] = acc;
+              else       pool[sm * PSS + 5 * 264 + cc * 33 + (rr0 + rrL) * 8] = acc;
             }
             __syncthreads();
           };
@@ -515,37 +629,48 @@
     }
 
     if (sweep == 1) {
-      if (tid == 0) vvec[0] = 1.0f;
+      if (tid < 2) vvec[tid * 36] = 1.0f;
       __syncthreads();
       for (int i = 0; i < 6; ++i) {
         const int ad = (i == 0) ? 1 : 4, bd = (i == 5) ? 1 : 4;
         const int adlog = (ad == 4) ? 2 : 0, bdlog = (bd == 4) ? 2 : 0;
         const int rows = g_ufin[i] * ad, cols = g_dfin[i] * bd;
         const int clog = 31 - __clz(cols);
-        const int ph = xi[i * 6 + 5];
         const float* tb = Tg + (size_t)(i * 6 + 5) * 512;
-        for (int e = tid; e < 256; e += BS) ATile[e] = tb[e * 2 + ph];
-        __syncthreads();
-        for (int e = tid; e < rows * cols; e += BS) {
+        for (int e2 = tid; e2 < 512; e2 += BS) {
+          const int sm = e2 >> 8, e = e2 & 255;
+          ATile[sm * 256 + e] = tb[e * 2 + xi[sm * 36 + i * 6 + 5]];
+        }
+        __syncthreads();
+        const int nel = rows * cols;
+        for (int e2 = tid; e2 < 2 * nel; e2 += BS) {
+          const int sm = (e2 >= nel) ? 1 : 0;
+          const int e = e2 - sm * nel;
           const int col = e & (cols - 1);
           const int ua = e >> clog;
           const int u = ua >> adlog, a = ua & (ad - 1);
           const int d_ = col >> bdlog, b = col & (bd - 1);
-          const float* fb = pool + i * 264 + u * 33 + d_;
-          const float4 av = *(const float4*)(ATile + a * 64 + b * 4);
-          GM[ua * 36 + col] = fb[0] * av.x + fb[8] * av.y + fb[16] * av.z + fb[24] * av.w;
-        }
-        __syncthreads();
-        if (tid < cols) {
+          const float* fb = pool + sm * PSS + i * 264 + u * 33 + d_;
+          const float4 av = *(const float4*)(ATile + sm * 256 + a * 64 + b * 4);
+          GM[sm * SS + ua * 36 + col] = fb[0] * av.x + fb[8] * av.y + fb[16] * av.z + fb[24] * av.w;
+        }
+        __syncthreads();
+        if (tid < 2 * cols) {
+          const int sm = (tid >= cols) ? 1 : 0;
+          const int c = tid - sm * cols;
           float acc = 0.f;
-          for (int r_ = 0; r_ < rows; ++r_) acc += vvec[r_] * GM[r_ * 36 + tid];
-          vvec2[tid] = acc;
-        }
-        __syncthreads();
-        if (tid < cols) vvec[tid] = vvec2[tid];
+          for (int r_ = 0; r_ < rows; ++r_) acc += vvec[sm * 36 + r_] * GM[sm * SS + r_ * 36 + c];
+          vvec2[sm * 36 + c] = acc;
+        }
+        __syncthreads();
+        if (tid < 2 * cols) {
+          const int sm = (tid >= cols) ? 1 : 0;
+          const int c = tid - sm * cols;
+          vvec[sm * 36 + c] = vvec2[sm * 36 + c];
+        }
         __syncthreads();
       }
-      if (tid == 0) out[s] = vvec[0];
+      if (tid < 2) out[s0 + tid] = vvec[tid * 36];
     }
   }
 }
@@ -564,5 +689,5 @@
   (void)in_sizes; (void)n_in; (void)out_size; (void)ws_size;
 
   mlp_kernel<<<dim3(128), dim3(256), 0, stream>>>(W1, b1, W2, b2, x, proj);
-  peps_kernel<<<dim3(1024), dim3(256), 0, stream>>>(Tg, x, proj, out);
-}
+  peps_kernel<<<dim3(512), dim3(256), 0, stream>>>(Tg, x, proj, out);
+}
```

Result: slower. 1.823 ms (+34.1%).
